# Kernel tuning notes

Measured on AMD Instinct MI355X. Metric: run time of the kernel, lower is better.

The kernel has to match this reference:

```python
import jax, jax.numpy as jnp
import numpy as np

B, T, N, L, D, H = 8, 6, 24, 1024, 512, 8
DH = D // H
EPS = 1e-5


def setup_inputs() -> dict:
    key = jax.random.key(0)
    ks = jax.random.split(key, 8)
    q = jax.random.normal(ks[0], (B, T, N, D), jnp.float32)
    k = jax.random.normal(ks[1], (B, T, L, D), jnp.float32)
    v = jax.random.normal(ks[2], (B, T, L, D), jnp.float32)
    attn_mask = jax.random.randint(ks[3], (T * N, T * L), 0, 10) == 0
    s = D ** -0.5
    Wq = jax.random.normal(ks[4], (D, D), jnp.float32) * s
    Wk = jax.random.normal(ks[5], (D, D), jnp.float32) * s
    Wv = jax.random.normal(ks[6], (D, D), jnp.float32) * s
    Wo = jax.random.normal(ks[7], (D, D), jnp.float32) * s
    return {"q": q, "k": k, "v": v, "attn_mask": attn_mask,
            "Wq": Wq, "Wk": Wk, "Wv": Wv, "Wo": Wo}


def reference(q, k, v, attn_mask, Wq, Wk, Wv, Wo):
    # Projections (torch Linear: y = x @ W.T), split into heads
    qp = (q.reshape(B, T * N, D) @ Wq.T).reshape(B, T * N, H, DH).transpose(0, 2, 1, 3)
    kp = (k.reshape(B, T * L, D) @ Wk.T).reshape(B, T * L, H, DH).transpose(0, 2, 1, 3)
    vp = (v.reshape(B, T * L, D) @ Wv.T).reshape(B, T * L, H, DH).transpose(0, 2, 1, 3)
    qp = qp * (DH ** -0.5)
    # scores: [B, H, T*N, T*L]
    scores = jnp.einsum('bhnd,bhmd->bhnm', qp, kp)
    scores = jnp.where(attn_mask[None, None], -jnp.inf, scores)
    # cross-head softmax: normalize over the combined (H*N) axis per (b, t, tl)
    a = scores.reshape(B, H, T, N, T * L).transpose(0, 2, 4, 1, 3)  # B,T,TL,H,N
    a = a.reshape(B, T, T * L, H * N)
    a = jax.nn.softmax(a, axis=-1)
    a = a.reshape(B, T, T * L, H, N).transpose(0, 3, 1, 4, 2).reshape(B, H, T * N, T * L)
    a = jnp.where(attn_mask[None, None], 0.0, a)
    attn_vis = a
    # renormalize along key axis
    a = a / (a.sum(axis=-1, keepdims=True) + EPS)
    out = jnp.einsum('bhnm,bhmd->bhnd', a, vp)  # B,H,T*N,DH
    out = out.transpose(0, 2, 1, 3).reshape(B, T * N, D)
    out = (out @ Wo.T).reshape(B, T, N, D)
    return out, attn_vis
```

## Files before the change

### kernel.cpp

```cpp
#include <hip/hip_runtime.h>
#include <hip/hip_bf16.h>
#include <math.h>

#define CB 8
#define CT 6
#define CN 24
#define CL 1024
#define CD 512
#define CH 8
#define CDH 64
#define CTN 144
#define CTL 6144
#define CMS 16
#define CEPS 1e-5f

typedef __bf16 bf16x8 __attribute__((ext_vector_type(8)));
typedef float  f32x4  __attribute__((ext_vector_type(4)));

#define MFMA16(a,b,c) __builtin_amdgcn_mfma_f32_16x16x32_bf16(a,b,c,0,0,0)

union BF8 { unsigned short s[8]; bf16x8 v; };

static __device__ __forceinline__ unsigned short f2bf(float x){
    union { float f; unsigned u; } c; c.f = x;
    return (unsigned short)((c.u + 0x7FFFu + ((c.u >> 16) & 1u)) >> 16);
}

static __device__ __forceinline__ float bf2f(unsigned short u){
    union { unsigned u; float f; } c; c.u = ((unsigned)u) << 16;
    return c.f;
}

static __device__ __forceinline__ bf16x8 cvt8(const float* __restrict__ p){
    const f32x4* q = (const f32x4*)p;
    f32x4 v0 = q[0], v1 = q[1];
    BF8 r;
    r.s[0]=f2bf(v0[0]); r.s[1]=f2bf(v0[1]); r.s[2]=f2bf(v0[2]); r.s[3]=f2bf(v0[3]);
    r.s[4]=f2bf(v1[0]); r.s[5]=f2bf(v1[1]); r.s[6]=f2bf(v1[2]); r.s[7]=f2bf(v1[3]);
    return r.v;
}

static __device__ __forceinline__ bf16x8 pack8(f32x4 a, f32x4 b){
    BF8 r;
    r.s[0]=f2bf(a[0]); r.s[1]=f2bf(a[1]); r.s[2]=f2bf(a[2]); r.s[3]=f2bf(a[3]);
    r.s[4]=f2bf(b[0]); r.s[5]=f2bf(b[1]); r.s[6]=f2bf(b[2]); r.s[7]=f2bf(b[3]);
    return r.v;
}

static __device__ __forceinline__ bf16x8 ldbf8(const unsigned short* __restrict__ p){
    return *(const bf16x8*)p;
}

#define GL16(gp, lp) __builtin_amdgcn_global_load_lds((const unsigned int*)(gp), (unsigned int*)(lp), 16, 0, 0)

__global__ void cvt_w_kernel(const float* __restrict__ w0, const float* __restrict__ w1,
                             const float* __restrict__ w2, const float* __restrict__ w3,
                             unsigned short* __restrict__ o0, unsigned short* __restrict__ o1,
                             unsigned short* __restrict__ o2, unsigned short* __restrict__ o3){
    int i = blockIdx.x*blockDim.x + threadIdx.x;
    const int n = CD*CD;
    if      (i < n)   o0[i]       = f2bf(w0[i]);
    else if (i < 2*n) o1[i-n]     = f2bf(w1[i-n]);
    else if (i < 3*n) o2[i-2*n]   = f2bf(w2[i-2*n]);
    else if (i < 4*n) o3[i-3*n]   = f2bf(w3[i-3*n]);
}

__global__ void maskb_kernel(const int* __restrict__ mask, unsigned int* __restrict__ maskb){
    int i = blockIdx.x*blockDim.x + threadIdx.x;
    if (i >= CT*CTL) return;
    int t = i / CTL, m = i - t*CTL;
    unsigned w = 0;
    for (int n = 0; n < 24; ++n)
        if (mask[(size_t)(t*24 + n)*CTL + m] != 0) w |= (1u << n);
    maskb[i] = w;
}

template<int MODE, int AFMT>
__global__ __launch_bounds__(512, 4) void gemm_m97(
    const void* __restrict__ Ap, const unsigned short* __restrict__ W,
    void* __restrict__ outv, int posPer, int rowoff, float scale)
{
    __shared__ union {
        struct { unsigned short As[128*64]; unsigned short Bs[128*64]; } s;
        float epi[32][129];
    } sm;

    int nwg = gridDim.x*gridDim.y;
    int id  = blockIdx.y*gridDim.x + blockIdx.x;
    int q8 = nwg >> 3, r8 = nwg & 7;
    int xcd = id & 7, rk = id >> 3;
    int swz = (xcd < r8 ? xcd*(q8+1) : r8*(q8+1) + (xcd-r8)*q8) + rk;
    int ctile = swz & 3;
    int bt    = swz >> 2;

    int tid = threadIdx.x;
    int lane = tid & 63, wave = tid >> 6;
    int wr = wave >> 2, wc = wave & 3;
    int qq = lane & 15, g = lane >> 4;

    int sr = tid >> 3;
    int sc = (((tid & 7) ^ ((sr >> 1) & 7)) * 8);
    const unsigned short* gah = (const unsigned short*)Ap + (size_t)(bt*128 + sr)*CD + sc;
    const unsigned short* gb  = W + (size_t)(ctile*128 + sr)*CD + sc;
    unsigned short* lA = sm.s.As + wave*512;
    unsigned short* lB = sm.s.Bs + wave*512;

    int arow = tid >> 2;
    const float* gaf = (const float*)Ap + (size_t)(bt*128 + arow)*CD + (tid & 3)*16;
    int akey = (arow >> 1) & 7;
    int asl0 = (tid & 3)*2;
    unsigned short* aw0 = sm.s.As + arow*64 + ((asl0     ^ akey)*8);
    unsigned short* aw1 = sm.s.As + arow*64 + (((asl0|1) ^ akey)*8);

    f32x4 acc[4][2] = {};
    int s1 = (qq >> 1) & 7;

    for (int k0 = 0; k0 < CD; k0 += 64) {
        if (AFMT == 0) {
            f32x4 w0 = *(const f32x4*)(gaf + k0);
            f32x4 w1 = *(const f32x4*)(gaf + k0 + 4);
            f32x4 w2 = *(const f32x4*)(gaf + k0 + 8);
            f32x4 w3 = *(const f32x4*)(gaf + k0 + 12);
            *(bf16x8*)aw0 = pack8(w0, w1);
            *(bf16x8*)aw1 = pack8(w2, w3);
        } else {
            GL16(gah + k0,          lA);
            GL16(gah + 64*CD + k0,  lA + 4096);
        }
        GL16(gb + k0,          lB);
        GL16(gb + 64*CD + k0,  lB + 4096);
        __syncthreads();
        #pragma unroll
        for (int x = 0; x < 2; ++x) {
            int slot = ((x*4 + g) ^ s1) * 8;
            bf16x8 af[4], bf[2];
            #pragma unroll
            for (int mf = 0; mf < 4; ++mf)
                af[mf] = *(const bf16x8*)&sm.s.As[(wr*64 + mf*16 + qq)*64 + slot];
            #pragma unroll
            for (int nf = 0; nf < 2; ++nf)
                bf[nf] = *(const bf16x8*)&sm.s.Bs[(wc*32 + nf*16 + qq)*64 + slot];
            #pragma unroll
            for (int mf = 0; mf < 4; ++mf)
                #pragma unroll
                for (int nf = 0; nf < 2; ++nf)
                    acc[mf][nf] = MFMA16(af[mf], bf[nf], acc[mf][nf]);
        }
        __syncthreads();
    }

    unsigned short* outu = (unsigned short*)outv;
    float* outf = (float*)outv;
    for (int p = 0; p < 4; ++p) {
        if (wr == (p >> 1)) {
            #pragma unroll
            for (int mh = 0; mh < 2; ++mh) {
                int mf = (p&1)*2 + mh;
                #pragma unroll
                for (int nf = 0; nf < 2; ++nf)
                    #pragma unroll
                    for (int r = 0; r < 4; ++r)
                        sm.epi[mh*16 + 4*g + r][wc*32 + nf*16 + qq] = acc[mf][nf][r]*scale;
            }
        }
        __syncthreads();
        if (MODE == 1) {
            #pragma unroll
            for (int i = 0; i < 8; ++i) {
                int c2 = i*16 + wave*2 + (lane>>5);
                int gr = rowoff + bt*128 + p*32 + (lane & 31);
                int bb = gr / posPer, pos = gr - bb*posPer;
                int hh = ctile*2 + (c2>>6), dh = c2 & 63;
                outu[((size_t)(bb*CH + hh)*64 + dh)*posPer + pos] = f2bf(sm.epi[lane&31][c2]);
            }
        } else {
            #pragma unroll
            for (int i = 0; i < 8; ++i) {
                int task = i*8 + wave;
                int lr = task >> 1, ch = task & 1;
                float val = sm.epi[lr][ch*64 + lane];
                int gr = rowoff + bt*128 + p*32 + lr;
                if (MODE == 2) {
                    outf[(size_t)gr*CD + ctile*128 + ch*64 + lane] = val;
                } else {
                    int bb = gr / posPer, pos = gr - bb*posPer;
                    int hh = ctile*2 + ch;
                    outu[((size_t)(bb*CH + hh)*posPer + pos)*64 + lane] = f2bf(val);
                }
            }
        }
        __syncthreads();
    }
}

__global__ __launch_bounds__(256) void scores_a_kernel(
    const unsigned short* __restrict__ qp, const unsigned short* __restrict__ kp,
    const unsigned int* __restrict__ maskb,
    float* __restrict__ pmax, float* __restrict__ psum)
{
    __shared__ float S[CTN][65];
    int mt = blockIdx.x;
    int h = blockIdx.y, b = blockIdx.z;
    int lane = threadIdx.x & 63, wave = threadIdx.x >> 6;
    const unsigned short* qbase = qp + (size_t)(b*CH + h)*CTN*64;
    const unsigned short* kbase = kp + (size_t)(b*CH + h)*CTL*64;
    int koff = 8*(lane>>4);
    f32x4 acc[3][4] = {};
    for (int k0 = 0; k0 < 64; k0 += 32) {
        bf16x8 bfr[4];
        #pragma unroll
        for (int cf = 0; cf < 4; ++cf)
            bfr[cf] = ldbf8(kbase + (size_t)(mt*64 + cf*16 + (lane&15))*64 + k0 + koff);
        #pragma unroll
        for (int i = 0; i < 3; ++i) {
            int rt = wave + 4*i;
            if (rt < 9) {
                bf16x8 a = ldbf8(qbase + (size_t)(rt*16 + (lane&15))*64 + k0 + koff);
                #pragma unroll
                for (int cf = 0; cf < 4; ++cf)
                    acc[i][cf] = MFMA16(a, bfr[cf], acc[i][cf]);
            }
        }
    }
    #pragma unroll
    for (int i = 0; i < 3; ++i) {
        int rt = wave + 4*i;
        if (rt < 9) {
            #pragma unroll
            for (int cf = 0; cf < 4; ++cf)
                #pragma unroll
                for (int r = 0; r < 4; ++r)
                    S[rt*16 + 4*(lane>>4) + r][cf*16 + (lane&15)] = acc[i][cf][r];
        }
    }
    __syncthreads();
    int mg0 = mt*64;
    for (int task = threadIdx.x; task < CT*64; task += 256) {
        int t = task >> 6, ml = task & 63;
        int mg = mg0 + ml;
        unsigned w = maskb[(size_t)t*CTL + mg];
        float mx = -INFINITY;
        float sv[24];
        #pragma unroll
        for (int i = 0; i < 24; ++i) {
            float s = ((w >> i) & 1u) ? -INFINITY : S[t*24 + i][ml];
            sv[i] = s;
            mx = fmaxf(mx, s);
        }
        float sum = 0.f;
        if (mx > -INFINITY) {
            #pragma unroll
            for (int i = 0; i < 24; ++i)
                if (sv[i] > -INFINITY) sum += __expf(sv[i] - mx);
        }
        size_t idx = ((size_t)(b*CH + h)*CT + t)*CTL + mg;
        pmax[idx] = mx; psum[idx] = sum;
    }
}

__global__ void combine_kernel(const float* __restrict__ pmax, const float* __restrict__ psum,
                               const unsigned int* __restrict__ maskb,
                               float2* __restrict__ stat2){
    size_t i = (size_t)blockIdx.x*blockDim.x + threadIdx.x;
    if (i >= (size_t)CB*CT*CTL) return;
    int m = (int)(i % CTL);
    size_t bt = i / CTL;
    int t = (int)(bt % CT), b = (int)(bt / CT);
    float pm[CH], ps[CH];
    float mx = -INFINITY;
    #pragma unroll
    for (int h = 0; h < CH; ++h) {
        size_t idx = ((size_t)(b*CH + h)*CT + t)*CTL + m;
        pm[h] = pmax[idx]; ps[h] = psum[idx];
        mx = fmaxf(mx, pm[h]);
    }
    float s = 0.f;
    if (mx > -INFINITY) {
        #pragma unroll
        for (int h = 0; h < CH; ++h)
            if (pm[h] > -INFINITY) s += ps[h]*__expf(pm[h] - mx);
    }
    float lse = (mx > -INFINITY && s > 0.f) ? mx + __logf(s) : 0.f;
    float2 o; o.x = lse; o.y = __uint_as_float(maskb[(size_t)t*CTL + m]);
    stat2[i] = o;
}

__global__ __launch_bounds__(64, 6) void fused_bpv(
    const unsigned short* __restrict__ qp, const unsigned short* __restrict__ kp,
    const unsigned short* __restrict__ vpT,
    const float2* __restrict__ stat2,
    float* __restrict__ avis, unsigned short* __restrict__ pvpart,
    float* __restrict__ rowpart)
{
    __shared__ unsigned short abf[16][68];
    __shared__ float av32[16][65];

    int ms = blockIdx.x;
    int rt = blockIdx.y;
    int bh = blockIdx.z;
    int b = bh >> 3;
    int lane = threadIdx.x;
    int qq = lane & 15, g = lane >> 4;
    int koff = 8*g;

    int qrow = rt*16 + qq;
    int t = qrow / 24;
    int rbit = qrow - t*24;

    const unsigned short* qbase = qp + (size_t)bh*CTN*64;
    const unsigned short* kbase = kp + (size_t)bh*CTL*64;
    const unsigned short* vb    = vpT + (size_t)bh*64*CTL;
    const float2* stp = stat2 + (size_t)(b*CT + t)*CTL;
    float* avbase = avis + ((size_t)bh*CTN + rt*16)*CTL;

    bf16x8 qf[2];
    #pragma unroll
    for (int x = 0; x < 2; ++x)
        qf[x] = ldbf8(qbase + (size_t)qrow*64 + x*32 + koff);

    f32x4 pv[4] = {};
    float rs = 0.f;

    for (int mt = 0; mt < 6; ++mt) {
        int mg0 = ms*384 + mt*64;
        bf16x8 vf[2][4];
        #pragma unroll
        for (int x = 0; x < 2; ++x)
            #pragma unroll
            for (int cf = 0; cf < 4; ++cf)
                vf[x][cf] = ldbf8(vb + (size_t)(cf*16 + qq)*CTL + mg0 + x*32 + koff);
        f32x4 sacc[4] = {};
        #pragma unroll
        for (int x = 0; x < 2; ++x) {
            bf16x8 kf[4];
            #pragma unroll
            for (int cf = 0; cf < 4; ++cf)
                kf[cf] = ldbf8(kbase + (size_t)(mg0 + cf*16 + qq)*64 + x*32 + koff);
            #pragma unroll
            for (int cf = 0; cf < 4; ++cf)
                sacc[cf] = MFMA16(kf[cf], qf[x], sacc[cf]);
        }
        #pragma unroll
        for (int cf = 0; cf < 4; ++cf) {
            const f32x4* sp = (const f32x4*)(stp + mg0 + cf*16 + 4*g);
            f32x4 s0 = sp[0], s1 = sp[1];
            f32x4 av;
            av[0] = ((__float_as_uint(s0[1]) >> rbit) & 1u) ? 0.f : __expf(sacc[cf][0] - s0[0]);
            av[1] = ((__float_as_uint(s0[3]) >> rbit) & 1u) ? 0.f : __expf(sacc[cf][1] - s0[2]);
            av[2] = ((__float_as_uint(s1[1]) >> rbit) & 1u) ? 0.f : __expf(sacc[cf][2] - s1[0]);
            av[3] = ((__float_as_uint(s1[3]) >> rbit) & 1u) ? 0.f : __expf(sacc[cf][3] - s1[2]);
            *(f32x4*)&av32[qq][cf*16 + 4*g] = av;
            unsigned short u4[4] = { f2bf(av[0]), f2bf(av[1]), f2bf(av[2]), f2bf(av[3]) };
            *(unsigned long long*)&abf[qq][cf*16 + 4*g] = *(unsigned long long*)u4;
            rs += av[0] + av[1] + av[2] + av[3];
        }
        #pragma unroll
        for (int p = 0; p < 4; ++p) {
            int row = 4*p + (lane >> 4);
            int col = 4*(lane & 15);
            f32x4 v4 = *(const f32x4*)&av32[row][col];
            __builtin_nontemporal_store(v4, (f32x4*)(avbase + (size_t)row*CTL + mg0 + col));
        }
        #pragma unroll
        for (int x = 0; x < 2; ++x) {
            bf16x8 af = *(const bf16x8*)&abf[qq][x*32 + koff];
            #pragma unroll
            for (int cf = 0; cf < 4; ++cf)
                pv[cf] = MFMA16(af, vf[x][cf], pv[cf]);
        }
    }

    rs += __shfl_xor(rs, 16);
    rs += __shfl_xor(rs, 32);
    if (g == 0)
        rowpart[(size_t)ms*(CB*CH*CTN) + (size_t)bh*CTN + qrow] = rs;
    unsigned short* pb = pvpart + ((size_t)(ms*64 + bh)*CTN + rt*16)*64;
    #pragma unroll
    for (int cf = 0; cf < 4; ++cf) {
        unsigned short u4[4] = { f2bf(pv[cf][0]), f2bf(pv[cf][1]), f2bf(pv[cf][2]), f2bf(pv[cf][3]) };
        *(unsigned long long*)&pb[cf*256 + lane*4] = *(unsigned long long*)u4;
    }
}

__global__ void pv_reduce_kernel(const unsigned short* __restrict__ pvpart,
                                 const float* __restrict__ rowpart,
                                 unsigned short* __restrict__ oh){
    int idx = blockIdx.x*blockDim.x + threadIdx.x;
    if (idx >= CB*CH*CTN*64) return;
    int col = idx & 63;
    int rowbh = idx >> 6;
    int row = rowbh % CTN, bh = rowbh / CTN;
    float rsum = 0.f;
    #pragma unroll
    for (int ms = 0; ms < CMS; ++ms)
        rsum += rowpart[(size_t)ms*(CB*CH*CTN) + rowbh];
    int rt = row >> 4, lr = row & 15, g = lr >> 2, r = lr & 3;
    int cf = col >> 4, qq = col & 15;
    size_t off = ((size_t)bh*CTN + rt*16)*64 + cf*256 + (g*16 + qq)*4 + r;
    float s = 0.f;
    #pragma unroll
    for (int ms = 0; ms < CMS; ++ms)
        s += bf2f(pvpart[(size_t)ms*((size_t)CB*CH*CTN*64) + off]);
    float inv = 1.f / (rsum + CEPS);
    int b = bh >> 3, h = bh & 7;
    oh[((size_t)b*CTN + row)*CD + h*64 + col] = f2bf(s*inv);
}

extern "C" void kernel_launch(void* const* d_in, const int* in_sizes, int n_in,
                              void* d_out, int out_size, void* d_ws, size_t ws_size,
                              hipStream_t stream)
{
    const float* q    = (const float*)d_in[0];
    const float* k    = (const float*)d_in[1];
    const float* v    = (const float*)d_in[2];
    const int*   mask = (const int*)  d_in[3];
    const float* Wq   = (const float*)d_in[4];
    const float* Wk   = (const float*)d_in[5];
    const float* Wv   = (const float*)d_in[6];
    const float* Wo   = (const float*)d_in[7];

    float* out0 = (float*)d_out;
    float* avis = out0 + (size_t)CB*CTN*CD;

    char* p = (char*)d_ws;
    auto alloc = [&](size_t bytes) -> char* {
        char* r = p; p += (bytes + 255) & ~(size_t)255; return r;
    };
    unsigned short* Wq_bf = (unsigned short*)alloc((size_t)CD*CD*2);
    unsigned short* Wk_bf = (unsigned short*)alloc((size_t)CD*CD*2);
    unsigned short* Wv_bf = (unsigned short*)alloc((size_t)CD*CD*2);
    unsigned short* Wo_bf = (unsigned short*)alloc((size_t)CD*CD*2);
    unsigned short* qp    = (unsigned short*)alloc((size_t)CB*CH*CTN*64*2);
    unsigned short* kp    = (unsigned short*)alloc((size_t)CB*CH*CTL*64*2);
    unsigned short* vpT   = (unsigned short*)alloc((size_t)CB*CH*64*CTL*2);
    char* S = alloc((size_t)CB*CH*CT*CTL*4*2);
    float* pmax   = (float*)S;
    float* psum   = (float*)(S + (size_t)CB*CH*CT*CTL*4);
    unsigned short* pvpart = (unsigned short*)S;
    float2* stat2 = (float2*)alloc((size_t)CB*CT*CTL*8);
    unsigned int* maskb = (unsigned int*)alloc((size_t)CT*CTL*4);
    float* rowpart = (float*)alloc((size_t)CMS*CB*CH*CTN*4);
    unsigned short* oh = (unsigned short*)alloc((size_t)CB*CTN*CD*2);

    cvt_w_kernel<<<(4*CD*CD + 255)/256, 256, 0, stream>>>(Wq, Wk, Wv, Wo,
                                                          Wq_bf, Wk_bf, Wv_bf, Wo_bf);
    maskb_kernel<<<(CT*CTL + 255)/256, 256, 0, stream>>>(mask, maskb);
    gemm_m97<0,0><<<dim3(4, CB*CTN/128), 512, 0, stream>>>(q, Wq_bf, qp, CTN, 0, 0.125f);
    for (int c = 0; c < 3; ++c)
        gemm_m97<0,0><<<dim3(4, 128), 512, 0, stream>>>(k + (size_t)c*16384*CD, Wk_bf, kp, CTL, c*16384, 1.0f);
    for (int c = 0; c < 3; ++c)
        gemm_m97<1,0><<<dim3(4, 128), 512, 0, stream>>>(v + (size_t)c*16384*CD, Wv_bf, vpT, CTL, c*16384, 1.0f);
    scores_a_kernel<<<dim3(CTL/64, CH, CB), 256, 0, stream>>>(qp, kp, maskb, pmax, psum);
    combine_kernel<<<((CB*CT*CTL) + 255)/256, 256, 0, stream>>>(pmax, psum, maskb, stat2);
    fused_bpv<<<dim3(CMS, 9, CB*CH), 64, 0, stream>>>(qp, kp, vpT, stat2,
                                                      avis, pvpart, rowpart);
    pv_reduce_kernel<<<((CB*CH*CTN*64) + 255)/256, 256, 0, stream>>>(pvpart, rowpart, oh);
    gemm_m97<2,1><<<dim3(4, CB*CTN/128), 512, 0, stream>>>(oh, Wo_bf, out0, CD, 0, 1.0f);
}
```

Before: 483.3 us.

## Process two query row tiles per fused_bpv block and merge K/V projection launches

Each fused_bpv block now handles two 16-row query tiles, so the K and V fragments loaded from global memory are reused across both tiles. The grid shrinks from 9 to 5 row groups, and the last group handles a single tile. Launch bounds drop to 3 blocks per SM to make room for the doubled accumulators. Separately, the three chunked K and V projection GEMM launches are each merged into one full-size launch, which reduces launch overhead. The costs are higher register pressure, lower occupancy and less parallelism in fused_bpv.

```diff
diff --git a/kernel.cpp b/kernel.cpp
--- a/kernel.cpp
+++ b/kernel.cpp
@@ -29,15 +29,6 @@
 static __device__ __forceinline__ float bf2f(unsigned short u){
     union { unsigned u; float f; } c; c.u = ((unsigned)u) << 16;
     return c.f;
-}
-
-static __device__ __forceinline__ bf16x8 cvt8(const float* __restrict__ p){
-    const f32x4* q = (const f32x4*)p;
-    f32x4 v0 = q[0], v1 = q[1];
-    BF8 r;
-    r.s[0]=f2bf(v0[0]); r.s[1]=f2bf(v0[1]); r.s[2]=f2bf(v0[2]); r.s[3]=f2bf(v0[3]);
-    r.s[4]=f2bf(v1[0]); r.s[5]=f2bf(v1[1]); r.s[6]=f2bf(v1[2]); r.s[7]=f2bf(v1[3]);
-    return r.v;
 }
 
 static __device__ __forceinline__ bf16x8 pack8(f32x4 a, f32x4 b){
@@ -285,7 +276,7 @@
     stat2[i] = o;
 }
 
-__global__ __launch_bounds__(64, 6) void fused_bpv(
+__global__ __launch_bounds__(64, 3) void fused_bpv(
     const unsigned short* __restrict__ qp, const unsigned short* __restrict__ kp,
     const unsigned short* __restrict__ vpT,
     const float2* __restrict__ stat2,
@@ -296,30 +287,39 @@
     __shared__ float av32[16][65];
 
     int ms = blockIdx.x;
-    int rt = blockIdx.y;
+    int ry = blockIdx.y;
     int bh = blockIdx.z;
     int b = bh >> 3;
     int lane = threadIdx.x;
     int qq = lane & 15, g = lane >> 4;
     int koff = 8*g;
-
-    int qrow = rt*16 + qq;
-    int t = qrow / 24;
-    int rbit = qrow - t*24;
+    int nrt = (ry < 4) ? 2 : 1;
+    int rt0 = ry*2;
 
     const unsigned short* qbase = qp + (size_t)bh*CTN*64;
     const unsigned short* kbase = kp + (size_t)bh*CTL*64;
     const unsigned short* vb    = vpT + (size_t)bh*64*CTL;
-    const float2* stp = stat2 + (size_t)(b*CT + t)*CTL;
-    float* avbase = avis + ((size_t)bh*CTN + rt*16)*CTL;
-
-    bf16x8 qf[2];
-    #pragma unroll
-    for (int x = 0; x < 2; ++x)
-        qf[x] = ldbf8(qbase + (size_t)qrow*64 + x*32 + koff);
-
-    f32x4 pv[4] = {};
-    float rs = 0.f;
+
+    int rbit[2];
+    const float2* stp[2];
+    float* avbase[2];
+    bf16x8 qf[2][2];
+    #pragma unroll
+    for (int i = 0; i < 2; ++i) {
+        int rt = rt0 + ((i < 2) ? i : 0);
+        if (i >= nrt) rt = rt0;
+        int qrow = rt*16 + qq;
+        int t = qrow / 24;
+        rbit[i] = qrow - t*24;
+        stp[i] = stat2 + (size_t)(b*CT + t)*CTL;
+        avbase[i] = avis + ((size_t)bh*CTN + rt*16)*CTL;
+        #pragma unroll
+        for (int x = 0; x < 2; ++x)
+            qf[i][x] = ldbf8(qbase + (size_t)qrow*64 + x*32 + koff);
+    }
+
+    f32x4 pv[2][4] = {};
+    float rs[2] = {0.f, 0.f};
 
     for (int mt = 0; mt < 6; ++mt) {
         int mg0 = ms*384 + mt*64;
@@ -329,7 +329,7 @@
             #pragma unroll
             for (int cf = 0; cf < 4; ++cf)
                 vf[x][cf] = ldbf8(vb + (size_t)(cf*16 + qq)*CTL + mg0 + x*32 + koff);
-        f32x4 sacc[4] = {};
+        f32x4 sacc[2][4] = {};
         #pragma unroll
         for (int x = 0; x < 2; ++x) {
             bf16x8 kf[4];
@@ -338,47 +338,65 @@
                 kf[cf] = ldbf8(kbase + (size_t)(mg0 + cf*16 + qq)*64 + x*32 + koff);
             #pragma unroll
             for (int cf = 0; cf < 4; ++cf)
-                sacc[cf] = MFMA16(kf[cf], qf[x], sacc[cf]);
-        }
-        #pragma unroll
-        for (int cf = 0; cf < 4; ++cf) {
-            const f32x4* sp = (const f32x4*)(stp + mg0 + cf*16 + 4*g);
-            f32x4 s0 = sp[0], s1 = sp[1];
-            f32x4 av;
-            av[0] = ((__float_as_uint(s0[1]) >> rbit) & 1u) ? 0.f : __expf(sacc[cf][0] - s0[0]);
-            av[1] = ((__float_as_uint(s0[3]) >> rbit) & 1u) ? 0.f : __expf(sacc[cf][1] - s0[2]);
-            av[2] = ((__float_as_uint(s1[1]) >> rbit) & 1u) ? 0.f : __expf(sacc[cf][2] - s1[0]);
-            av[3] = ((__float_as_uint(s1[3]) >> rbit) & 1u) ? 0.f : __expf(sacc[cf][3] - s1[2]);
-            *(f32x4*)&av32[qq][cf*16 + 4*g] = av;
-            unsigned short u4[4] = { f2bf(av[0]), f2bf(av[1]), f2bf(av[2]), f2bf(av[3]) };
-            *(unsigned long long*)&abf[qq][cf*16 + 4*g] = *(unsigned long long*)u4;
-            rs += av[0] + av[1] + av[2] + av[3];
-        }
-        #pragma unroll
-        for (int p = 0; p < 4; ++p) {
-            int row = 4*p + (lane >> 4);
-            int col = 4*(lane & 15);
-            f32x4 v4 = *(const f32x4*)&av32[row][col];
-            __builtin_nontemporal_store(v4, (f32x4*)(avbase + (size_t)row*CTL + mg0 + col));
-        }
-        #pragma unroll
-        for (int x = 0; x < 2; ++x) {
-            bf16x8 af = *(const bf16x8*)&abf[qq][x*32 + koff];
-            #pragma unroll
-            for (int cf = 0; cf < 4; ++cf)
-                pv[cf] = MFMA16(af, vf[x][cf], pv[cf]);
-        }
-    }
-
-    rs += __shfl_xor(rs, 16);
-    rs += __shfl_xor(rs, 32);
-    if (g == 0)
-        rowpart[(size_t)ms*(CB*CH*CTN) + (size_t)bh*CTN + qrow] = rs;
-    unsigned short* pb = pvpart + ((size_t)(ms*64 + bh)*CTN + rt*16)*64;
-    #pragma unroll
-    for (int cf = 0; cf < 4; ++cf) {
-        unsigned short u4[4] = { f2bf(pv[cf][0]), f2bf(pv[cf][1]), f2bf(pv[cf][2]), f2bf(pv[cf][3]) };
-        *(unsigned long long*)&pb[cf*256 + lane*4] = *(unsigned long long*)u4;
+                sacc[0][cf] = MFMA16(kf[cf], qf[0][x], sacc[0][cf]);
+            if (nrt == 2) {
+                #pragma unroll
+                for (int cf = 0; cf < 4; ++cf)
+                    sacc[1][cf] = MFMA16(kf[cf], qf[1][x], sacc[1][cf]);
+            }
+        }
+        #pragma unroll
+        for (int i = 0; i < 2; ++i) {
+            if (i < nrt) {
+                #pragma unroll
+                for (int cf = 0; cf < 4; ++cf) {
+                    const f32x4* sp = (const f32x4*)(stp[i] + mg0 + cf*16 + 4*g);
+                    f32x4 s0 = sp[0], s1 = sp[1];
+                    f32x4 av;
+                    av[0] = ((__float_as_uint(s0[1]) >> rbit[i]) & 1u) ? 0.f : __expf(sacc[i][cf][0] - s0[0]);
+                    av[1] = ((__float_as_uint(s0[3]) >> rbit[i]) & 1u) ? 0.f : __expf(sacc[i][cf][1] - s0[2]);
+                    av[2] = ((__float_as_uint(s1[1]) >> rbit[i]) & 1u) ? 0.f : __expf(sacc[i][cf][2] - s1[0]);
+                    av[3] = ((__float_as_uint(s1[3]) >> rbit[i]) & 1u) ? 0.f : __expf(sacc[i][cf][3] - s1[2]);
+                    *(f32x4*)&av32[qq][cf*16 + 4*g] = av;
+                    unsigned short u4[4] = { f2bf(av[0]), f2bf(av[1]), f2bf(av[2]), f2bf(av[3]) };
+                    *(unsigned long long*)&abf[qq][cf*16 + 4*g] = *(unsigned long long*)u4;
+                    rs[i] += av[0] + av[1] + av[2] + av[3];
+                }
+                #pragma unroll
+                for (int p = 0; p < 4; ++p) {
+                    int row = 4*p + (lane >> 4);
+                    int col = 4*(lane & 15);
+                    f32x4 v4 = *(const f32x4*)&av32[row][col];
+                    __builtin_nontemporal_store(v4, (f32x4*)(avbase[i] + (size_t)row*CTL + mg0 + col));
+                }
+                #pragma unroll
+                for (int x = 0; x < 2; ++x) {
+                    bf16x8 af = *(const bf16x8*)&abf[qq][x*32 + koff];
+                    #pragma unroll
+                    for (int cf = 0; cf < 4; ++cf)
+                        pv[i][cf] = MFMA16(af, vf[x][cf], pv[i][cf]);
+                }
+            }
+        }
+    }
+
+    #pragma unroll
+    for (int i = 0; i < 2; ++i) {
+        if (i < nrt) {
+            int rt = rt0 + i;
+            float s = rs[i];
+            s += __shfl_xor(s, 16);
+            s += __shfl_xor(s, 32);
+            if (g == 0)
+                rowpart[(size_t)ms*(CB*CH*CTN) + (size_t)bh*CTN + rt*16 + qq] = s;
+            unsigned short* pb = pvpart + ((size_t)(ms*64 + bh)*CTN + rt*16)*64;
+            #pragma unroll
+            for (int cf = 0; cf < 4; ++cf) {
+                unsigned short u4[4] = { f2bf(pv[i][cf][0]), f2bf(pv[i][cf][1]),
+                                         f2bf(pv[i][cf][2]), f2bf(pv[i][cf][3]) };
+                *(unsigned long long*)&pb[cf*256 + lane*4] = *(unsigned long long*)u4;
+            }
+        }
     }
 }
 
@@ -446,13 +464,11 @@
                                                           Wq_bf, Wk_bf, Wv_bf, Wo_bf);
     maskb_kernel<<<(CT*CTL + 255)/256, 256, 0, stream>>>(mask, maskb);
     gemm_m97<0,0><<<dim3(4, CB*CTN/128), 512, 0, stream>>>(q, Wq_bf, qp, CTN, 0, 0.125f);
-    for (int c = 0; c < 3; ++c)
-        gemm_m97<0,0><<<dim3(4, 128), 512, 0, stream>>>(k + (size_t)c*16384*CD, Wk_bf, kp, CTL, c*16384, 1.0f);
-    for (int c = 0; c < 3; ++c)
-        gemm_m97<1,0><<<dim3(4, 128), 512, 0, stream>>>(v + (size_t)c*16384*CD, Wv_bf, vpT, CTL, c*16384, 1.0f);
+    gemm_m97<0,0><<<dim3(4, CB*CTL/128), 512, 0, stream>>>(k, Wk_bf, kp, CTL, 0, 1.0f);
+    gemm_m97<1,0><<<dim3(4, CB*CTL/128), 512, 0, stream>>>(v, Wv_bf, vpT, CTL, 0, 1.0f);
     scores_a_kernel<<<dim3(CTL/64, CH, CB), 256, 0, stream>>>(qp, kp, maskb, pmax, psum);
     combine_kernel<<<((CB*CT*CTL) + 255)/256, 256, 0, stream>>>(pmax, psum, maskb, stat2);
-    fused_bpv<<<dim3(CMS, 9, CB*CH), 64, 0, stream>>>(qp, kp, vpT, stat2,
+    fused_bpv<<<dim3(CMS, 5, CB*CH), 64, 0, stream>>>(qp, kp, vpT, stat2,
                                                       avis, pvpart, rowpart);
     pv_reduce_kernel<<<((CB*CH*CTN*64) + 255)/256, 256, 0, stream>>>(pvpart, rowpart, oh);
     gemm_m97<2,1><<<dim3(4, CB*CTN/128), 512, 0, stream>>>(oh, Wo_bf, out0, CD, 0, 1.0f);
```

Measured after the change: 436.7 us. -9.6%, faster.
